# Kernel tuning notes

Hardware: AMD Instinct MI355X
Metric: run time of the kernel (lower is better)

## Reference

```python
import jax, jax.numpy as jnp
import numpy as np

EMBED = 3072
HEADS = 24
HEAD_DIM = EMBED // HEADS
FFN = 4 * EMBED
SEGS = (1024, 2048, 4096)
DILS = (1, 2, 4)
SEQ = 8192
BATCH = 1


def setup_inputs() -> dict:
    key = jax.random.key(0)
    ks = jax.random.split(key, 8)
    E, F = EMBED, FFN
    s = lambda k, shape, sc: (jax.random.normal(k, shape, jnp.float32) * sc)
    return {
        "x": s(ks[0], (BATCH, SEQ, E), 1.0),
        "expert_embed": s(ks[1], (1, 1, E), 0.02),
        "w_qkv": s(ks[2], (3 * E, E), E ** -0.5),
        "b_qkv": jnp.zeros((3 * E,), jnp.float32),
        "w_out": s(ks[3], (E, E), E ** -0.5),
        "b_out": jnp.zeros((E,), jnp.float32),
        "ln1_g": jnp.ones((E,), jnp.float32),
        "ln1_b": jnp.zeros((E,), jnp.float32),
        "w1": s(ks[4], (F, E), E ** -0.5),
        "b1": jnp.zeros((F,), jnp.float32),
        "w2": s(ks[5], (E, F), F ** -0.5),
        "b2": jnp.zeros((E,), jnp.float32),
        "ln2_g": jnp.ones((E,), jnp.float32),
        "ln2_b": jnp.zeros((E,), jnp.float32),
    }


def _layernorm(x, g, b):
    m = jnp.mean(x, axis=-1, keepdims=True)
    v = jnp.mean(jnp.square(x - m), axis=-1, keepdims=True)
    return (x - m) * jax.lax.rsqrt(v + 1e-5) * g + b


def _dilated_attn(q, k, v):
    # q,k,v: [b, n, h, d]; heads are partitioned across dilation groups
    b, n, h, d = q.shape
    G = len(SEGS)
    hg = h // G
    scale = 1.0 / np.sqrt(d)
    outs = []
    for i, (g, r) in enumerate(zip(SEGS, DILS)):
        off = i % r
        hs = slice(i * hg, (i + 1) * hg)

        def sel(t):
            # [b, n, h, d] -> [b, n//g, g//r, hg, d] (dilated segment view)
            return t.reshape(b, n // g, g, h, d)[:, :, off::r, hs, :]

        qi, ki, vi = sel(q), sel(k), sel(v)
        att = jnp.einsum("bsqhd,bskhd->bshqk", qi, ki) * scale
        att = jax.nn.softmax(att, axis=-1)
        oi = jnp.einsum("bshqk,bskhd->bsqhd", att, vi)
        # scatter dilated positions back; unselected positions stay zero
        buf = jnp.zeros((b, n // g, g, hg, d), q.dtype).at[:, :, off::r].set(oi)
        outs.append(buf.reshape(b, n, hg, d))
    return jnp.concatenate(outs, axis=2)  # head groups are contiguous slices


def reference(x, expert_embed, w_qkv, b_qkv, w_out, b_out,
              ln1_g, ln1_b, w1, b1, w2, b2, ln2_g, ln2_b):
    b, n, E = x.shape
    x = x + expert_embed
    qkv = x @ w_qkv.T + b_qkv
    q, k, v = [t.reshape(b, n, HEADS, HEAD_DIM) for t in jnp.split(qkv, 3, axis=-1)]
    a = _dilated_attn(q, k, v).reshape(b, n, E) @ w_out.T + b_out
    x = _layernorm(x + a, ln1_g, ln1_b)
    f = jax.nn.gelu(x @ w1.T + b1, approximate=False) @ w2.T + b2
    return _layernorm(x + f, ln2_g, ln2_b)
```

## Files before the change

### kernel.cpp

```cpp
#include <hip/hip_runtime.h>

typedef unsigned short u16;
typedef __bf16 bf16x8 __attribute__((ext_vector_type(8)));
typedef float f32x4 __attribute__((ext_vector_type(4)));
typedef u16 u16x4 __attribute__((ext_vector_type(4)));
typedef u16 u16x8 __attribute__((ext_vector_type(8)));

__device__ __forceinline__ u16 f2bf(float f) {
  union { float f; unsigned u; } v; v.f = f;
  return (u16)((v.u + 0x7fffu + ((v.u >> 16) & 1u)) >> 16);
}
__device__ __forceinline__ float b2f(u16 h) {
  union { unsigned u; float f; } v; v.u = ((unsigned)h) << 16; return v.f;
}

__device__ __forceinline__ void gld16(const void* g, void* l) {
  __builtin_amdgcn_global_load_lds(
      (const __attribute__((address_space(1))) unsigned int*)g,
      (__attribute__((address_space(3))) unsigned int*)l, 16, 0, 0);
}

#define BAR() asm volatile("s_barrier" ::: "memory")
#define VMC6() asm volatile("s_waitcnt vmcnt(6)" ::: "memory")
#define VMC0() asm volatile("s_waitcnt vmcnt(0)" ::: "memory")

__global__ __launch_bounds__(256) void prep_kernel(const float* __restrict__ x,
                                                   const float* __restrict__ ee,
                                                   u16* __restrict__ xb) {
  size_t i = ((size_t)blockIdx.x * 256 + threadIdx.x) * 4;
  int col = (int)(i % 3072);
  f32x4 v = *(const f32x4*)&x[i];
  f32x4 e = *(const f32x4*)&ee[col];
  v += e;
  u16x4 b = { f2bf(v[0]), f2bf(v[1]), f2bf(v[2]), f2bf(v[3]) };
  *(u16x4*)&xb[i] = b;
}

__global__ __launch_bounds__(256) void cvt_kernel(const float* __restrict__ in,
                                                  u16* __restrict__ out, size_t n) {
  size_t i = ((size_t)blockIdx.x * 256 + threadIdx.x) * 4;
  if (i >= n) return;
  f32x4 v = *(const f32x4*)&in[i];
  u16x4 b = { f2bf(v[0]), f2bf(v[1]), f2bf(v[2]), f2bf(v[3]) };
  *(u16x4*)&out[i] = b;
}

__global__ __launch_bounds__(256) void cvt_strided_kernel(const float* __restrict__ in,
                                                          u16* __restrict__ out, int k0) {
  size_t i = ((size_t)blockIdx.x * 256 + threadIdx.x) * 4;
  int n = (int)(i / 6144), k = (int)(i % 6144);
  f32x4 v = *(const f32x4*)&in[(size_t)n * 12288 + k0 + k];
  u16x4 b = { f2bf(v[0]), f2bf(v[1]), f2bf(v[2]), f2bf(v[3]) };
  *(u16x4*)&out[i] = b;
}

template<int EPI>
__global__ __launch_bounds__(512, 2) void gemm8_kernel(const u16* __restrict__ A,
                                                       const u16* __restrict__ B,
                                                       const float* __restrict__ bias,
                                                       void* __restrict__ C0,
                                                       void* __restrict__ C1,
                                                       int N, int K) {
  __shared__ __align__(16) u16 lds[65536];
  const int tid = threadIdx.x;
  const int lane = tid & 63;
  const int w = tid >> 6;
  const int lr = lane & 15, lc8 = (lane >> 4) * 8;
  const int wm128 = (w >> 2) * 128, wn64 = (w & 3) * 64;
  const int rsw = (lr & 7) << 3;

  const int ntile = N >> 8;
  int bid = blockIdx.x;
  int wg = (bid & 7) * (gridDim.x >> 3) + (bid >> 3);
  const int bm = wg / ntile, bn = wg % ntile;
  const size_t m0 = (size_t)bm << 8, n0 = (size_t)bn << 8;

  const int jsw = (tid & 7) ^ ((tid >> 3) & 7);
  const u16* gA = A + (m0 + (tid >> 3)) * (size_t)K + jsw * 8;
  const u16* gB = B + (n0 + ((tid >> 8) << 6) + ((tid >> 3) & 31)) * (size_t)K + jsw * 8;
  u16* lA = &lds[tid * 8];
  u16* lB = &lds[16384 + (((tid >> 8) << 12) | (((tid >> 3) & 31) << 6) | ((tid & 7) << 3))];

  f32x4 acc[8][4] = {};
  bf16x8 af[2][4], bfr[2][2];

  auto stageA = [&](int buf, int mh, int kk) {
    const int ro = mh * 64;
    gld16(gA + (size_t)ro * K + kk, lA + buf * 32768 + ro * 64);
    gld16(gA + (size_t)(ro + 128) * K + kk, lA + buf * 32768 + (ro + 128) * 64);
  };
  auto stageB = [&](int buf, int nh, int kk) {
    const int ro = nh * 32;
    gld16(gB + (size_t)ro * K + kk, lB + buf * 32768 + ro * 64);
    gld16(gB + (size_t)(ro + 128) * K + kk, lB + buf * 32768 + (ro + 128) * 64);
  };
  auto LA = [&](int buf, int mh) {
#pragma unroll
    for (int ks = 0; ks < 2; ++ks)
#pragma unroll
      for (int f = 0; f < 4; ++f) {
        int r = wm128 + mh * 64 + f * 16 + lr;
        af[ks][f] = *(const bf16x8*)&lds[buf * 32768 + r * 64 + ((ks * 32 + lc8) ^ rsw)];
      }
  };
  auto LB = [&](int buf, int nh) {
#pragma unroll
    for (int ks = 0; ks < 2; ++ks)
#pragma unroll
      for (int f = 0; f < 2; ++f) {
        int r = wn64 + nh * 32 + f * 16 + lr;
        bfr[ks][f] = *(const bf16x8*)&lds[buf * 32768 + 16384 + r * 64 + ((ks * 32 + lc8) ^ rsw)];
      }
  };
  auto MMA = [&](int mh, int nh) {
    __builtin_amdgcn_s_setprio(1);
#pragma unroll
    for (int ks = 0; ks < 2; ++ks)
#pragma unroll
      for (int f = 0; f < 4; ++f)
#pragma unroll
        for (int f2 = 0; f2 < 2; ++f2)
          acc[mh * 4 + f][nh * 2 + f2] = __builtin_amdgcn_mfma_f32_16x16x32_bf16(
              af[ks][f], bfr[ks][f2], acc[mh * 4 + f][nh * 2 + f2], 0, 0, 0);
    __builtin_amdgcn_s_setprio(0);
  };

  stageA(0, 0, 0); stageB(0, 1, 0); stageA(0, 1, 0); stageB(0, 0, 0);
  stageA(1, 0, 64); stageB(1, 1, 64); stageA(1, 1, 64);
  VMC6();
  BAR();

  const int NIT = K >> 7;
  for (int it = 0; it < NIT; ++it) {
    const int kk = it << 7;
    const bool pred = (it + 1 < NIT);
    LA(0, 0); LB(0, 0);
    stageB(1, 0, kk + 64);
    BAR(); MMA(0, 0); BAR();
    LB(0, 1);
    if (pred) stageA(0, 0, kk + 128);
    BAR(); MMA(0, 1); BAR();
    LA(0, 1);
    if (pred) stageB(0, 1, kk + 128);
    BAR(); MMA(1, 1); BAR();
    LB(0, 0);
    if (pred) stageA(0, 1, kk + 128);
    BAR(); MMA(1, 0);
    if (pred) { VMC6(); } else { VMC0(); }
    BAR();
    LA(1, 0); LB(1, 0);
    if (pred) stageB(0, 0, kk + 128);
    BAR(); MMA(0, 0); BAR();
    LB(1, 1);
    if (pred) stageA(1, 0, kk + 192);
    BAR(); MMA(0, 1); BAR();
    LA(1, 1);
    if (pred) stageB(1, 1, kk + 192);
    BAR(); MMA(1, 1); BAR();
    LB(1, 0);
    if (pred) stageA(1, 1, kk + 192);
    BAR(); MMA(1, 0);
    if (pred) { VMC6(); }
    BAR();
  }

#pragma unroll
  for (int ni = 0; ni < 4; ++ni) {
    const int colL = wn64 + ni * 16 + lr;
    const size_t col = n0 + colL;
    const float bv = bias[col];
    const int ci = colL >> 3;
#pragma unroll
    for (int mi = 0; mi < 8; ++mi) {
#pragma unroll
      for (int rg = 0; rg < 4; ++rg) {
        const int rowL = wm128 + mi * 16 + (lc8 >> 1) + rg;
        float v = acc[mi][ni][rg] + bv;
        if constexpr (EPI == 2)
          v = 0.5f * v * (1.0f + erff(v * 0.7071067811865476f));
        const int fz = (rowL >> 2) & 7;
        lds[rowL * 256 + (((ci ^ fz) << 3) | (colL & 7))] = f2bf(v);
      }
    }
  }
  __syncthreads();
  const int row = tid >> 1, half = tid & 1;
  const int fro = (row >> 2) & 7;
  u16* dst;
  size_t cb;
  int ldc;
  if constexpr (EPI == 7) {
    const int sec = (n0 >= 3072);
    dst = sec ? (u16*)C1 : (u16*)C0;
    cb = n0 - (sec ? 3072 : 0);
    ldc = 3072;
  } else {
    dst = (u16*)C0; cb = n0; ldc = N;
  }
  u16* gout = dst + (m0 + row) * (size_t)ldc + cb + half * 128;
#pragma unroll
  for (int i = 0; i < 16; ++i) {
    const int ci = half * 16 + i;
    *(uint4*)&gout[i * 8] = *(const uint4*)&lds[row * 256 + ((ci ^ fro) << 3)];
  }
}

template<int EPI>
__global__ __launch_bounds__(512, 2) void gemm4p_kernel(const u16* __restrict__ A,
                                                        const u16* __restrict__ B,
                                                        const float* __restrict__ bias,
                                                        const float* __restrict__ residf,
                                                        const u16* __restrict__ residb,
                                                        const float* __restrict__ ee,
                                                        void* __restrict__ C0,
                                                        int N, int K) {
  __shared__ __align__(16) u16 lds[73728];
  const int tid = threadIdx.x;
  const int lane = tid & 63;
  const int w = tid >> 6;
  const int lr = lane & 15, lc8 = (lane >> 4) * 8;
  const int wm64 = (w >> 1) * 64;
  const int wn64 = (w & 1) * 64;
  const int rsw = (lr & 7) << 3;

  const int ntile = N >> 7;
  int bid = blockIdx.x;
  int wg = (bid & 7) * (gridDim.x >> 3) + (bid >> 3);
  const int bm = wg / ntile, bn = wg % ntile;
  const size_t m0 = (size_t)bm << 8, n0 = (size_t)bn << 7;

  const int jsw = (tid & 7) ^ ((tid >> 3) & 7);
  const u16* gA = A + (m0 + (tid >> 3)) * (size_t)K + jsw * 8;
  const u16* gB = B + (n0 + (tid >> 3)) * (size_t)K + jsw * 8;
  u16* lA = &lds[tid * 8];
  u16* lB = &lds[16384 + tid * 8];

  f32x4 acc[4][4] = {};
  bf16x8 af[2][4], bfr[2][2];

  const int NT = K >> 6;

  auto stageA2 = [&](int buf, int kk) {
    gld16(gA + kk, lA + buf * 24576);
    gld16(gA + (size_t)128 * K + kk, lA + buf * 24576 + 128 * 64);
    gld16(gA + (size_t)64 * K + kk, lA + buf * 24576 + 64 * 64);
    gld16(gA + (size_t)192 * K + kk, lA + buf * 24576 + 192 * 64);
  };
  auto stageB1 = [&](int buf, int kk) {
    gld16(gB + kk, lB + buf * 24576);
    gld16(gB + (size_t)64 * K + kk, lB + buf * 24576 + 64 * 64);
  };
  auto LA = [&](int buf) {
#pragma unroll
    for (int ks = 0; ks < 2; ++ks)
#pragma unroll
      for (int f = 0; f < 4; ++f) {
        int r = wm64 + f * 16 + lr;
        af[ks][f] = *(const bf16x8*)&lds[buf * 24576 + r * 64 + ((ks * 32 + lc8) ^ rsw)];
      }
  };
  auto LB = [&](int buf, int ch) {
#pragma unroll
    for (int ks = 0; ks < 2; ++ks)
#pragma unroll
      for (int f2 = 0; f2 < 2; ++f2) {
        int r = wn64 + ch * 32 + f2 * 16 + lr;
        bfr[ks][f2] = *(const bf16x8*)&lds[buf * 24576 + 16384 + r * 64 + ((ks * 32 + lc8) ^ rsw)];
      }
  };
  auto MMA = [&](int ch) {
    __builtin_amdgcn_s_setprio(1);
#pragma unroll
    for (int ks = 0; ks < 2; ++ks)
#pragma unroll
      for (int f = 0; f < 4; ++f)
#pragma unroll
        for (int f2 = 0; f2 < 2; ++f2)
          acc[f][ch * 2 + f2] = __builtin_amdgcn_mfma_f32_16x16x32_bf16(
              af[ks][f], bfr[ks][f2], acc[f][ch * 2 + f2], 0, 0, 0);
    __builtin_amdgcn_s_setprio(0);
  };
  auto TILE = [&](int bc, int bs, int tt) {
    const int kk2 = (tt + 2) << 6;
    const bool p = (tt + 2) < NT;
    LA(bc); LB(bc, 0);
    if (p) stageA2(bs, kk2);
    BAR(); MMA(0); BAR();
    LB(bc, 1);
    if (p) stageB1(bs, kk2);
    BAR(); MMA(1);
    if (p) { VMC6(); } else { VMC0(); }
    BAR();
  };

  stageA2(0, 0); stageB1(0, 0);
  stageA2(1, 64); stageB1(1, 64);
  VMC6();
  BAR();

  for (int t = 0; t < NT; t += 3) {
    TILE(0, 2, t);
    TILE(1, 0, t + 1);
    TILE(2, 1, t + 2);
  }

#pragma unroll
  for (int nf = 0; nf < 4; ++nf) {
    const int colL = wn64 + nf * 16 + lr;
    const size_t col = n0 + colL;
    float bv = 0.f;
    if constexpr (EPI != 9) bv = bias[col];
    const int ci = colL >> 3;
#pragma unroll
    for (int f = 0; f < 4; ++f) {
#pragma unroll
      for (int rg = 0; rg < 4; ++rg) {
        const int rowL = wm64 + f * 16 + (lc8 >> 1) + rg;
        const size_t idx = (m0 + rowL) * (size_t)N + col;
        float v = acc[f][nf][rg] + bv;
        if constexpr (EPI == 3) v += residf[idx] + ee[col];
        if constexpr (EPI == 8) v += b2f(residb[idx]);
        if constexpr (EPI == 9) v += b2f(((const u16*)C0)[idx]);
        const int fz = (rowL >> 2) & 7;
        lds[rowL * 128 + (((ci ^ fz) << 3) | (colL & 7))] = f2bf(v);
      }
    }
  }
  __syncthreads();
  const int row = tid >> 1, half = tid & 1;
  const int fro = (row >> 2) & 7;
  u16* gout = (u16*)C0 + (m0 + row) * (size_t)N + n0 + half * 64;
#pragma unroll
  for (int i = 0; i < 8; ++i) {
    const int ci = half * 8 + i;
    *(uint4*)&gout[i * 8] = *(const uint4*)&lds[row * 128 + ((ci ^ fro) << 3)];
  }
}

__device__ __forceinline__ void decode_blk(int bid, int& grp, int& g, int& r, int& off,
                                           int& q16, int& hl, int& s) {
  if (bid < 1024)      { grp = 0; g = 1024; r = 1; off = 0; }
  else if (bid < 1536) { grp = 1; g = 2048; r = 2; off = 1; bid -= 1024; }
  else                 { grp = 2; g = 4096; r = 4; off = 2; bid -= 1536; }
  q16 = bid & 15; hl = (bid >> 4) & 7; s = bid >> 7;
}

__global__ __launch_bounds__(256) void vtrans_kernel(const u16* __restrict__ Vb,
                                                     u16* __restrict__ vtd) {
  int grp, g, r, off, jb, hl, s;
  decode_blk(blockIdx.x, grp, g, r, off, jb, hl, s);
  const int h = grp * 8 + hl;
  const size_t vbase = (size_t)((grp == 0) ? 0u : (grp == 1) ? 8388608u : 12582912u)
                       + (size_t)(s * 8 + hl) * 131072;
  __shared__ u16 t[64 * 128];
  const int tid = threadIdx.x;
#pragma unroll
  for (int i = 0; i < 4; ++i) {
    int c = tid + i * 256;
    int jj = c >> 4, c16 = c & 15;
    size_t pos = (size_t)s * g + off + (size_t)(jb * 64 + jj) * r;
    uint4 d = *(const uint4*)&Vb[pos * 3072 + h * 128 + c16 * 8];
    *(uint4*)((char*)t + jj * 256 + ((c16 * 16) ^ ((jj >> 3) << 4))) = d;
  }
  __syncthreads();
#pragma unroll
  for (int i = 0; i < 4; ++i) {
    int c = tid + i * 256;
    int dd = c >> 3, jc = c & 7;
    u16x8 vals;
#pragma unroll
    for (int q = 0; q < 8; ++q) {
      int row = jc * 8 + q;
      vals[q] = *(const u16*)((const char*)t + row * 256 + ((dd * 2) ^ (jc << 4)));
    }
    *(u16x8*)&vtd[vbase + (size_t)dd * 1024 + jb * 64 + jc * 8] = vals;
  }
}

__global__ __launch_bounds__(256) void attn_kernel(const u16* __restrict__ Qb,
                                                   const u16* __restrict__ Kb,
                                                   const u16* __restrict__ vtd,
                                                   u16* __restrict__ abuf) {
  int grp, g, r, off, qt, hl, s;
  decode_blk(blockIdx.x, grp, g, r, off, qt, hl, s);
  const int h = grp * 8 + hl;
  const size_t vbase = (size_t)((grp == 0) ? 0u : (grp == 1) ? 8388608u : 12582912u)
                       + (size_t)(s * 8 + hl) * 131072;
  const size_t segoff = (size_t)s * g + off;

  const int tid = threadIdx.x;
  const int lane = tid & 63, w = tid >> 6;
  const int lr = lane & 15, lc = lane >> 4;

  __shared__ u16 Kl[64 * 128];
  __shared__ u16 Vl[128 * 64];
  __shared__ u16 Pl[4][1024];

  const size_t qpos = segoff + (size_t)(qt * 64 + w * 16 + lr) * r;
  const u16* qrow = &Qb[qpos * 3072 + h * 128];
  bf16x8 qf[4];
#pragma unroll
  for (int kc = 0; kc < 4; ++kc) qf[kc] = *(const bf16x8*)&qrow[kc * 32 + lc * 8];

  float m_run[4], l_run[4];
  f32x4 ao[8] = {};
#pragma unroll
  for (int i = 0; i < 4; ++i) { m_run[i] = -1e30f; l_run[i] = 0.f; }

  const float scale = 0.08838834764831845f;

  for (int kt = 0; kt < 16; ++kt) {
    __syncthreads();
#pragma unroll
    for (int i = 0; i < 4; ++i) {
      int c = tid + i * 256;
      int jj = c >> 4, c16 = c & 15;
      size_t kpos = segoff + (size_t)(kt * 64 + jj) * r;
      uint4 kd = *(const uint4*)&Kb[kpos * 3072 + h * 128 + c16 * 8];
      *(uint4*)((char*)Kl + jj * 256 + ((c16 * 16) ^ ((jj & 7) << 4))) = kd;
      int dd = c >> 3, jc = c & 7;
      uint4 vd = *(const uint4*)&vtd[vbase + (size_t)dd * 1024 + kt * 64 + jc * 8];
      *(uint4*)((char*)Vl + dd * 128 + ((jc * 16) ^ ((dd & 7) << 4))) = vd;
    }
    __syncthreads();

    f32x4 sc4[4] = {};
#pragma unroll
    for (int kb = 0; kb < 4; ++kb) {
      const int key = kb * 16 + lr;
      const int swz = (key & 7) << 4;
#pragma unroll
      for (int kc = 0; kc < 4; ++kc) {
        bf16x8 kf = *(const bf16x8*)((const char*)Kl + key * 256 + ((kc * 64 + lc * 16) ^ swz));
        sc4[kb] = __builtin_amdgcn_mfma_f32_16x16x32_bf16(qf[kc], kf, sc4[kb], 0, 0, 0);
      }
    }

    float pv[4][4];
#pragma unroll
    for (int rg = 0; rg < 4; ++rg) {
      float t = fmaxf(fmaxf(sc4[0][rg], sc4[1][rg]), fmaxf(sc4[2][rg], sc4[3][rg]));
#pragma unroll
      for (int sh = 1; sh < 16; sh <<= 1) t = fmaxf(t, __shfl_xor(t, sh, 64));
      t *= scale;
      const float mn = fmaxf(m_run[rg], t);
      const float corr = __expf(m_run[rg] - mn);
      m_run[rg] = mn;
      float sum = 0.f;
#pragma unroll
      for (int kb = 0; kb < 4; ++kb) {
        float p = __expf(sc4[kb][rg] * scale - mn);
        pv[kb][rg] = p; sum += p;
      }
#pragma unroll
      for (int sh = 1; sh < 16; sh <<= 1) sum += __shfl_xor(sum, sh, 64);
      l_run[rg] = l_run[rg] * corr + sum;
#pragma unroll
      for (int nb = 0; nb < 8; ++nb) ao[nb][rg] *= corr;
    }

#pragma unroll
    for (int rg = 0; rg < 4; ++rg) {
      const int q = lc * 4 + rg;
      const int swq = (q & 7) << 4;
#pragma unroll
      for (int kb = 0; kb < 4; ++kb) {
        const int key = kb * 16 + lr;
        *(u16*)((char*)&Pl[w][0] + q * 128 + ((key * 2) ^ swq)) = f2bf(pv[kb][rg]);
      }
    }
    __syncthreads();

#pragma unroll
    for (int kc2 = 0; kc2 < 2; ++kc2) {
      bf16x8 pf = *(const bf16x8*)((const char*)&Pl[w][0] + lr * 128 + ((kc2 * 64 + lc * 16) ^ ((lr & 7) << 4)));
#pragma unroll
      for (int nb = 0; nb < 8; ++nb) {
        const int dd = nb * 16 + lr;
        bf16x8 vf = *(const bf16x8*)((const char*)Vl + dd * 128 + ((kc2 * 64 + lc * 16) ^ ((dd & 7) << 4)));
        ao[nb] = __builtin_amdgcn_mfma_f32_16x16x32_bf16(pf, vf, ao[nb], 0, 0, 0);
      }
    }
  }

#pragma unroll
  for (int rg = 0; rg < 4; ++rg) {
    const float inv = 1.f / l_run[rg];
    const size_t opos = segoff + (size_t)(qt * 64 + w * 16 + lc * 4 + rg) * r;
    u16* orow = &abuf[opos * 3072 + h * 128];
#pragma unroll
    for (int nb = 0; nb < 8; ++nb) orow[nb * 16 + lr] = f2bf(ao[nb][rg] * inv);
  }
}

template<int IN_BF, int OUT_BF>
__global__ __launch_bounds__(256) void ln_kernel(const void* __restrict__ yv,
                                                 const float* __restrict__ gm,
                                                 const float* __restrict__ bt,
                                                 void* __restrict__ outv) {
  const size_t row = blockIdx.x;
  const int tid = threadIdx.x;
  float v[12];
  float s = 0.f, ss = 0.f;
#pragma unroll
  for (int i = 0; i < 3; ++i) {
    if constexpr (IN_BF) {
      u16x4 raw = *(const u16x4*)((const u16*)yv + row * 3072 + tid * 4 + i * 1024);
#pragma unroll
      for (int j = 0; j < 4; ++j) { float f = b2f(raw[j]); v[i * 4 + j] = f; s += f; ss += f * f; }
    } else {
      f32x4 raw = *(const f32x4*)((const float*)yv + row * 3072 + tid * 4 + i * 1024);
#pragma unroll
      for (int j = 0; j < 4; ++j) { float f = raw[j]; v[i * 4 + j] = f; s += f; ss += f * f; }
    }
  }
#pragma unroll
  for (int sh = 1; sh < 64; sh <<= 1) { s += __shfl_xor(s, sh, 64); ss += __shfl_xor(ss, sh, 64); }
  __shared__ float red[8];
  if ((tid & 63) == 0) { red[tid >> 6] = s; red[4 + (tid >> 6)] = ss; }
  __syncthreads();
  s = red[0] + red[1] + red[2] + red[3];
  ss = red[4] + red[5] + red[6] + red[7];
  const float mean = s * (1.f / 3072.f);
  const float var = ss * (1.f / 3072.f) - mean * mean;
  const float rs = rsqrtf(var + 1e-5f);
#pragma unroll
  for (int i = 0; i < 3; ++i) {
    int c = tid * 4 + i * 1024;
    f32x4 g4 = *(const f32x4*)&gm[c];
    f32x4 b4 = *(const f32x4*)&bt[c];
    if constexpr (OUT_BF) {
      u16x4 ob;
#pragma unroll
      for (int j = 0; j < 4; ++j) ob[j] = f2bf((v[i * 4 + j] - mean) * rs * g4[j] + b4[j]);
      *(u16x4*)((u16*)outv + row * 3072 + c) = ob;
    } else {
      f32x4 o;
#pragma unroll
      for (int j = 0; j < 4; ++j) o[j] = (v[i * 4 + j] - mean) * rs * g4[j] + b4[j];
      *(f32x4*)((float*)outv + row * 3072 + c) = o;
    }
  }
}

extern "C" void kernel_launch(void* const* d_in, const int* in_sizes, int n_in,
                              void* d_out, int out_size, void* d_ws, size_t ws_size,
                              hipStream_t stream) {
  (void)in_sizes; (void)n_in; (void)out_size;
  const float* x    = (const float*)d_in[0];
  const float* ee   = (const float*)d_in[1];
  const float* wqkv = (const float*)d_in[2];
  const float* bqkv = (const float*)d_in[3];
  const float* wout = (const float*)d_in[4];
  const float* bout = (const float*)d_in[5];
  const float* ln1g = (const float*)d_in[6];
  const float* ln1b = (const float*)d_in[7];
  const float* w1   = (const float*)d_in[8];
  const float* b1   = (const float*)d_in[9];
  const float* w2   = (const float*)d_in[10];
  const float* b2   = (const float*)d_in[11];
  const float* ln2g = (const float*)d_in[12];
  const float* ln2b = (const float*)d_in[13];
  float* out = (float*)d_out;

  static const size_t OFF_B1  = 50331648;
  static const size_t OFF_B2  = 100663296;
  static const size_t WS_NEED = 150994944;
  if (ws_size < WS_NEED) return;

  char* ws = (char*)d_ws;
  u16*   xb    = (u16*)(ws);
  u16*   vtd   = (u16*)(ws);
  u16*   wbo   = (u16*)(ws);
  u16*   x1b   = (u16*)(ws);
  u16*   Qb    = (u16*)(ws + OFF_B1);
  u16*   y1b   = (u16*)(ws + OFF_B1);
  u16*   y2b   = (u16*)(ws + OFF_B1);
  u16*   wslot = (u16*)(ws + OFF_B2);
  u16*   abuf  = (u16*)(ws + OFF_B2);
  u16*   Kb    = (u16*)d_out;
  u16*   Vb    = (u16*)((char*)d_out + 50331648);
  u16*   hcd   = (u16*)d_out;

  prep_kernel<<<24576, 256, 0, stream>>>(x, ee, xb);

  cvt_kernel<<<18432, 256, 0, stream>>>(wqkv, wslot, 18874368);
  gemm8_kernel<7><<<768, 512, 0, stream>>>(xb, wslot, bqkv, Qb, Kb, 6144, 3072);
  cvt_kernel<<<9216, 256, 0, stream>>>(wqkv + 18874368, wslot, 9437184);
  gemm4p_kernel<0><<<768, 512, 0, stream>>>(xb, wslot, bqkv + 6144, nullptr, nullptr, nullptr,
                                            Vb, 3072, 3072);

  vtrans_kernel<<<1792, 256, 0, stream>>>(Vb, vtd);
  hipMemsetAsync(abuf, 0, 50331648, stream);
  attn_kernel<<<1792, 256, 0, stream>>>(Qb, Kb, vtd, abuf);

  cvt_kernel<<<9216, 256, 0, stream>>>(wout, wbo, 9437184);
  gemm4p_kernel<3><<<768, 512, 0, stream>>>(abuf, wbo, bout, x, nullptr, ee,
                                            y1b, 3072, 3072);
  ln_kernel<1, 1><<<8192, 256, 0, stream>>>(y1b, ln1g, ln1b, x1b);

  for (int c = 0; c < 2; ++c) {
    cvt_kernel<<<18432, 256, 0, stream>>>(w1 + (size_t)c * 18874368, wslot, 18874368);
    gemm8_kernel<2><<<768, 512, 0, stream>>>(x1b, wslot, b1 + c * 6144, hcd, nullptr, 6144, 3072);
    cvt_strided_kernel<<<18432, 256, 0, stream>>>(w2, wslot, c * 6144);
    if (c == 0)
      gemm4p_kernel<8><<<768, 512, 0, stream>>>(hcd, wslot, b2, nullptr, x1b, nullptr,
                                                y2b, 3072, 6144);
    else
      gemm4p_kernel<9><<<768, 512, 0, stream>>>(hcd, wslot, b2, nullptr, nullptr, nullptr,
                                                y2b, 3072, 6144);
  }

  ln_kernel<1, 0><<<8192, 256, 0, stream>>>(y2b, ln2g, ln2b, out);
}
```

Before: 2.253 ms.

## Restructure GEMM pipelines to load full B fragment and halve barrier phases

Both GEMM kernels now load the whole per-wave B fragment at once and issue larger MFMA blocks per phase. This halves the number of barrier-separated sub-steps per K-tile, and the staging order and vmcnt waits are reorganised to match. In the 256x256 kernel the LDS layout moves to separate A and B regions. The goal is to cut barrier and LDS-read scheduling overhead, at the cost of more live fragment registers and a changed pipeline depth that could expose memory latency or create races.

```diff
diff --git a/kernel.cpp b/kernel.cpp
--- a/kernel.cpp
+++ b/kernel.cpp
@@ -21,7 +21,9 @@
 }
 
 #define BAR() asm volatile("s_barrier" ::: "memory")
+#define VMC8() asm volatile("s_waitcnt vmcnt(8)" ::: "memory")
 #define VMC6() asm volatile("s_waitcnt vmcnt(6)" ::: "memory")
+#define VMC2() asm volatile("s_waitcnt vmcnt(2)" ::: "memory")
 #define VMC0() asm volatile("s_waitcnt vmcnt(0)" ::: "memory")
 
 __global__ __launch_bounds__(256) void prep_kernel(const float* __restrict__ x,
@@ -79,20 +81,20 @@
   const u16* gA = A + (m0 + (tid >> 3)) * (size_t)K + jsw * 8;
   const u16* gB = B + (n0 + ((tid >> 8) << 6) + ((tid >> 3) & 31)) * (size_t)K + jsw * 8;
   u16* lA = &lds[tid * 8];
-  u16* lB = &lds[16384 + (((tid >> 8) << 12) | (((tid >> 3) & 31) << 6) | ((tid & 7) << 3))];
+  u16* lB = &lds[32768 + (((tid >> 8) << 12) | (((tid >> 3) & 31) << 6) | ((tid & 7) << 3))];
 
   f32x4 acc[8][4] = {};
-  bf16x8 af[2][4], bfr[2][2];
+  bf16x8 af[2][4], bfr[2][4];
 
   auto stageA = [&](int buf, int mh, int kk) {
     const int ro = mh * 64;
-    gld16(gA + (size_t)ro * K + kk, lA + buf * 32768 + ro * 64);
-    gld16(gA + (size_t)(ro + 128) * K + kk, lA + buf * 32768 + (ro + 128) * 64);
+    gld16(gA + (size_t)ro * K + kk, lA + buf * 16384 + ro * 64);
+    gld16(gA + (size_t)(ro + 128) * K + kk, lA + buf * 16384 + (ro + 128) * 64);
   };
   auto stageB = [&](int buf, int nh, int kk) {
     const int ro = nh * 32;
-    gld16(gB + (size_t)ro * K + kk, lB + buf * 32768 + ro * 64);
-    gld16(gB + (size_t)(ro + 128) * K + kk, lB + buf * 32768 + (ro + 128) * 64);
+    gld16(gB + (size_t)ro * K + kk, lB + buf * 16384 + ro * 64);
+    gld16(gB + (size_t)(ro + 128) * K + kk, lB + buf * 16384 + (ro + 128) * 64);
   };
   auto LA = [&](int buf, int mh) {
 #pragma unroll
@@ -100,67 +102,58 @@
 #pragma unroll
       for (int f = 0; f < 4; ++f) {
         int r = wm128 + mh * 64 + f * 16 + lr;
-        af[ks][f] = *(const bf16x8*)&lds[buf * 32768 + r * 64 + ((ks * 32 + lc8) ^ rsw)];
-      }
-  };
-  auto LB = [&](int buf, int nh) {
+        af[ks][f] = *(const bf16x8*)&lds[buf * 16384 + r * 64 + ((ks * 32 + lc8) ^ rsw)];
+      }
+  };
+  auto LBall = [&](int buf) {
 #pragma unroll
     for (int ks = 0; ks < 2; ++ks)
 #pragma unroll
-      for (int f = 0; f < 2; ++f) {
-        int r = wn64 + nh * 32 + f * 16 + lr;
-        bfr[ks][f] = *(const bf16x8*)&lds[buf * 32768 + 16384 + r * 64 + ((ks * 32 + lc8) ^ rsw)];
-      }
-  };
-  auto MMA = [&](int mh, int nh) {
+      for (int f = 0; f < 4; ++f) {
+        int r = wn64 + f * 16 + lr;
+        bfr[ks][f] = *(const bf16x8*)&lds[32768 + buf * 16384 + r * 64 + ((ks * 32 + lc8) ^ rsw)];
+      }
+  };
+  auto MMA = [&](int mh) {
     __builtin_amdgcn_s_setprio(1);
 #pragma unroll
     for (int ks = 0; ks < 2; ++ks)
 #pragma unroll
       for (int f = 0; f < 4; ++f)
 #pragma unroll
-        for (int f2 = 0; f2 < 2; ++f2)
-          acc[mh * 4 + f][nh * 2 + f2] = __builtin_amdgcn_mfma_f32_16x16x32_bf16(
-              af[ks][f], bfr[ks][f2], acc[mh * 4 + f][nh * 2 + f2], 0, 0, 0);
+        for (int f2 = 0; f2 < 4; ++f2)
+          acc[mh * 4 + f][f2] = __builtin_amdgcn_mfma_f32_16x16x32_bf16(
+              af[ks][f], bfr[ks][f2], acc[mh * 4 + f][f2], 0, 0, 0);
     __builtin_amdgcn_s_setprio(0);
   };
 
-  stageA(0, 0, 0); stageB(0, 1, 0); stageA(0, 1, 0); stageB(0, 0, 0);
-  stageA(1, 0, 64); stageB(1, 1, 64); stageA(1, 1, 64);
-  VMC6();
+  stageB(0, 0, 0); stageB(0, 1, 0); stageA(0, 0, 0);
+  stageA(0, 1, 0);
+  stageB(1, 0, 64); stageB(1, 1, 64); stageA(1, 0, 64);
+  VMC8();
   BAR();
 
   const int NIT = K >> 7;
   for (int it = 0; it < NIT; ++it) {
     const int kk = it << 7;
     const bool pred = (it + 1 < NIT);
-    LA(0, 0); LB(0, 0);
-    stageB(1, 0, kk + 64);
-    BAR(); MMA(0, 0); BAR();
-    LB(0, 1);
-    if (pred) stageA(0, 0, kk + 128);
-    BAR(); MMA(0, 1); BAR();
+    LBall(0); LA(0, 0);
+    stageA(1, 1, kk + 64);
+    BAR(); MMA(0); VMC8(); BAR();
     LA(0, 1);
-    if (pred) stageB(0, 1, kk + 128);
-    BAR(); MMA(1, 1); BAR();
-    LB(0, 0);
+    if (pred) { stageB(0, 0, kk + 128); stageB(0, 1, kk + 128); stageA(0, 0, kk + 128); }
+    BAR(); MMA(1);
+    if (pred) { VMC8(); } else { VMC2(); }
+    BAR();
+    LBall(1); LA(1, 0);
     if (pred) stageA(0, 1, kk + 128);
-    BAR(); MMA(1, 0);
-    if (pred) { VMC6(); } else { VMC0(); }
+    BAR(); MMA(0);
+    if (pred) { VMC8(); } else { VMC0(); }
     BAR();
-    LA(1, 0); LB(1, 0);
-    if (pred) stageB(0, 0, kk + 128);
-    BAR(); MMA(0, 0); BAR();
-    LB(1, 1);
-    if (pred) stageA(1, 0, kk + 192);
-    BAR(); MMA(0, 1); BAR();
     LA(1, 1);
-    if (pred) stageB(1, 1, kk + 192);
-    BAR(); MMA(1, 1); BAR();
-    LB(1, 0);
-    if (pred) stageA(1, 1, kk + 192);
-    BAR(); MMA(1, 0);
-    if (pred) { VMC6(); }
+    if (pred) { stageB(1, 0, kk + 192); stageB(1, 1, kk + 192); stageA(1, 0, kk + 192); }
+    BAR(); MMA(1);
+    if (pred) { VMC8(); }
     BAR();
   }
 
@@ -206,7 +199,7 @@
 }
 
 template<int EPI>
-__global__ __launch_bounds__(512, 2) void gemm4p_kernel(const u16* __restrict__ A,
+__global__ __launch_bounds__(512, 2) void gemm1p_kernel(const u16* __restrict__ A,
                                                         const u16* __restrict__ B,
                                                         const float* __restrict__ bias,
                                                         const float* __restrict__ residf,
@@ -236,17 +229,17 @@
   u16* lB = &lds[16384 + tid * 8];
 
   f32x4 acc[4][4] = {};
-  bf16x8 af[2][4], bfr[2][2];
+  bf16x8 af[2][4], bfr[2][4];
 
   const int NT = K >> 6;
 
   auto stageA2 = [&](int buf, int kk) {
     gld16(gA + kk, lA + buf * 24576);
+    gld16(gA + (size_t)64 * K + kk, lA + buf * 24576 + 64 * 64);
     gld16(gA + (size_t)128 * K + kk, lA + buf * 24576 + 128 * 64);
-    gld16(gA + (size_t)64 * K + kk, lA + buf * 24576 + 64 * 64);
     gld16(gA + (size_t)192 * K + kk, lA + buf * 24576 + 192 * 64);
   };
-  auto stageB1 = [&](int buf, int kk) {
+  auto stageB2 = [&](int buf, int kk) {
     gld16(gB + kk, lB + buf * 24576);
     gld16(gB + (size_t)64 * K + kk, lB + buf * 24576 + 64 * 64);
   };
@@ -259,42 +252,39 @@
         af[ks][f] = *(const bf16x8*)&lds[buf * 24576 + r * 64 + ((ks * 32 + lc8) ^ rsw)];
       }
   };
-  auto LB = [&](int buf, int ch) {
+  auto LBall = [&](int buf) {
 #pragma unroll
     for (int ks = 0; ks < 2; ++ks)
 #pragma unroll
-      for (int f2 = 0; f2 < 2; ++f2) {
-        int r = wn64 + ch * 32 + f2 * 16 + lr;
-        bfr[ks][f2] = *(const bf16x8*)&lds[buf * 24576 + 16384 + r * 64 + ((ks * 32 + lc8) ^ rsw)];
-      }
-  };
-  auto MMA = [&](int ch) {
+      for (int f = 0; f < 4; ++f) {
+        int r = wn64 + f * 16 + lr;
+        bfr[ks][f] = *(const bf16x8*)&lds[buf * 24576 + 16384 + r * 64 + ((ks * 32 + lc8) ^ rsw)];
+      }
+  };
+  auto MMA = [&]() {
     __builtin_amdgcn_s_setprio(1);
 #pragma unroll
     for (int ks = 0; ks < 2; ++ks)
 #pragma unroll
       for (int f = 0; f < 4; ++f)
 #pragma unroll
-        for (int f2 = 0; f2 < 2; ++f2)
-          acc[f][ch * 2 + f2] = __builtin_amdgcn_mfma_f32_16x16x32_bf16(
-              af[ks][f], bfr[ks][f2], acc[f][ch * 2 + f2], 0, 0, 0);
+        for (int f2 = 0; f2 < 4; ++f2)
+          acc[f][f2] = __builtin_amdgcn_mfma_f32_16x16x32_bf16(
+              af[ks][f], bfr[ks][f2], acc[f][f2], 0, 0, 0);
     __builtin_amdgcn_s_setprio(0);
   };
   auto TILE = [&](int bc, int bs, int tt) {
     const int kk2 = (tt + 2) << 6;
     const bool p = (tt + 2) < NT;
-    LA(bc); LB(bc, 0);
-    if (p) stageA2(bs, kk2);
-    BAR(); MMA(0); BAR();
-    LB(bc, 1);
-    if (p) stageB1(bs, kk2);
-    BAR(); MMA(1);
+    LA(bc); LBall(bc);
+    if (p) { stageA2(bs, kk2); stageB2(bs, kk2); }
+    BAR(); MMA();
     if (p) { VMC6(); } else { VMC0(); }
     BAR();
   };
 
-  stageA2(0, 0); stageB1(0, 0);
-  stageA2(1, 64); stageB1(1, 64);
+  stageA2(0, 0); stageB2(0, 0);
+  stageA2(1, 64); stageB2(1, 64);
   VMC6();
   BAR();
 
@@ -587,7 +577,7 @@
   cvt_kernel<<<18432, 256, 0, stream>>>(wqkv, wslot, 18874368);
   gemm8_kernel<7><<<768, 512, 0, stream>>>(xb, wslot, bqkv, Qb, Kb, 6144, 3072);
   cvt_kernel<<<9216, 256, 0, stream>>>(wqkv + 18874368, wslot, 9437184);
-  gemm4p_kernel<0><<<768, 512, 0, stream>>>(xb, wslot, bqkv + 6144, nullptr, nullptr, nullptr,
+  gemm1p_kernel<0><<<768, 512, 0, stream>>>(xb, wslot, bqkv + 6144, nullptr, nullptr, nullptr,
                                             Vb, 3072, 3072);
 
   vtrans_kernel<<<1792, 256, 0, stream>>>(Vb, vtd);
@@ -595,7 +585,7 @@
   attn_kernel<<<1792, 256, 0, stream>>>(Qb, Kb, vtd, abuf);
 
   cvt_kernel<<<9216, 256, 0, stream>>>(wout, wbo, 9437184);
-  gemm4p_kernel<3><<<768, 512, 0, stream>>>(abuf, wbo, bout, x, nullptr, ee,
+  gemm1p_kernel<3><<<768, 512, 0, stream>>>(abuf, wbo, bout, x, nullptr, ee,
                                             y1b, 3072, 3072);
   ln_kernel<1, 1><<<8192, 256, 0, stream>>>(y1b, ln1g, ln1b, x1b);
 
@@ -604,10 +594,10 @@
     gemm8_kernel<2><<<768, 512, 0, stream>>>(x1b, wslot, b1 + c * 6144, hcd, nullptr, 6144, 3072);
     cvt_strided_kernel<<<18432, 256, 0, stream>>>(w2, wslot, c * 6144);
     if (c == 0)
-      gemm4p_kernel<8><<<768, 512, 0, stream>>>(hcd, wslot, b2, nullptr, x1b, nullptr,
+      gemm1p_kernel<8><<<768, 512, 0, stream>>>(hcd, wslot, b2, nullptr, x1b, nullptr,
                                                 y2b, 3072, 6144);
     else
-      gemm4p_kernel<9><<<768, 512, 0, stream>>>(hcd, wslot, b2, nullptr, nullptr, nullptr,
+      gemm1p_kernel<9><<<768, 512, 0, stream>>>(hcd, wslot, b2, nullptr, nullptr, nullptr,
                                                 y2b, 3072, 6144);
   }
 
```

New measurement: 2.318 ms. 2.9% more time.

## Merge split MMA phases in 4-phase GEMM and reorder gemm8 prefetch schedule

Applied to the files above, without the earlier changes.

The 256x128 GEMM now loads all B fragments per k-tile and issues a single MMA block with one barrier per tile instead of two half-tile phases separated by barriers. The 8-wave GEMM reorders which A/B stages are prefetched in each phase and tightens the vmcnt wait from 6 to 4 outstanding loads. The aim is to cut barrier stalls and better align global loads with their consumers. Costs are higher register pressure from the larger B fragment array and less interleaving of LDS reads with MFMA work.

```diff
diff --git a/kernel.cpp b/kernel.cpp
--- a/kernel.cpp
+++ b/kernel.cpp
@@ -21,6 +21,7 @@
 }
 
 #define BAR() asm volatile("s_barrier" ::: "memory")
+#define VMC4() asm volatile("s_waitcnt vmcnt(4)" ::: "memory")
 #define VMC6() asm volatile("s_waitcnt vmcnt(6)" ::: "memory")
 #define VMC0() asm volatile("s_waitcnt vmcnt(0)" ::: "memory")
 
@@ -126,8 +127,8 @@
   };
 
   stageA(0, 0, 0); stageB(0, 1, 0); stageA(0, 1, 0); stageB(0, 0, 0);
-  stageA(1, 0, 64); stageB(1, 1, 64); stageA(1, 1, 64);
-  VMC6();
+  stageA(1, 0, 64); stageB(1, 1, 64);
+  VMC4();
   BAR();
 
   const int NIT = K >> 7;
@@ -135,32 +136,32 @@
     const int kk = it << 7;
     const bool pred = (it + 1 < NIT);
     LA(0, 0); LB(0, 0);
-    stageB(1, 0, kk + 64);
+    stageA(1, 1, kk + 64);
     BAR(); MMA(0, 0); BAR();
     LB(0, 1);
-    if (pred) stageA(0, 0, kk + 128);
+    stageB(1, 0, kk + 64);
     BAR(); MMA(0, 1); BAR();
     LA(0, 1);
-    if (pred) stageB(0, 1, kk + 128);
+    if (pred) stageA(0, 0, kk + 128);
     BAR(); MMA(1, 1); BAR();
     LB(0, 0);
-    if (pred) stageA(0, 1, kk + 128);
+    if (pred) stageB(0, 1, kk + 128);
     BAR(); MMA(1, 0);
-    if (pred) { VMC6(); } else { VMC0(); }
+    if (pred) { VMC4(); } else { VMC0(); }
     BAR();
     LA(1, 0); LB(1, 0);
-    if (pred) stageB(0, 0, kk + 128);
+    if (pred) stageA(0, 1, kk + 128);
     BAR(); MMA(0, 0); BAR();
     LB(1, 1);
-    if (pred) stageA(1, 0, kk + 192);
+    if (pred) stageB(0, 0, kk + 128);
     BAR(); MMA(0, 1); BAR();
     LA(1, 1);
-    if (pred) stageB(1, 1, kk + 192);
+    if (pred) stageA(1, 0, kk + 192);
     BAR(); MMA(1, 1); BAR();
     LB(1, 0);
-    if (pred) stageA(1, 1, kk + 192);
+    if (pred) stageB(1, 1, kk + 192);
     BAR(); MMA(1, 0);
-    if (pred) { VMC6(); }
+    if (pred) { VMC4(); }
     BAR();
   }
 
@@ -206,14 +207,14 @@
 }
 
 template<int EPI>
-__global__ __launch_bounds__(512, 2) void gemm4p_kernel(const u16* __restrict__ A,
-                                                        const u16* __restrict__ B,
-                                                        const float* __restrict__ bias,
-                                                        const float* __restrict__ residf,
-                                                        const u16* __restrict__ residb,
-                                                        const float* __restrict__ ee,
-                                                        void* __restrict__ C0,
-                                                        int N, int K) {
+__global__ __launch_bounds__(512, 2) void gemmu_kernel(const u16* __restrict__ A,
+                                                       const u16* __restrict__ B,
+                                                       const float* __restrict__ bias,
+                                                       const float* __restrict__ residf,
+                                                       const u16* __restrict__ residb,
+                                                       const float* __restrict__ ee,
+                                                       void* __restrict__ C0,
+                                                       int N, int K) {
   __shared__ __align__(16) u16 lds[73728];
   const int tid = threadIdx.x;
   const int lane = tid & 63;
@@ -236,17 +237,17 @@
   u16* lB = &lds[16384 + tid * 8];
 
   f32x4 acc[4][4] = {};
-  bf16x8 af[2][4], bfr[2][2];
+  bf16x8 af[2][4], bfr[2][4];
 
   const int NT = K >> 6;
 
   auto stageA2 = [&](int buf, int kk) {
     gld16(gA + kk, lA + buf * 24576);
+    gld16(gA + (size_t)64 * K + kk, lA + buf * 24576 + 64 * 64);
     gld16(gA + (size_t)128 * K + kk, lA + buf * 24576 + 128 * 64);
-    gld16(gA + (size_t)64 * K + kk, lA + buf * 24576 + 64 * 64);
     gld16(gA + (size_t)192 * K + kk, lA + buf * 24576 + 192 * 64);
   };
-  auto stageB1 = [&](int buf, int kk) {
+  auto stageB2 = [&](int buf, int kk) {
     gld16(gB + kk, lB + buf * 24576);
     gld16(gB + (size_t)64 * K + kk, lB + buf * 24576 + 64 * 64);
   };
@@ -259,42 +260,39 @@
         af[ks][f] = *(const bf16x8*)&lds[buf * 24576 + r * 64 + ((ks * 32 + lc8) ^ rsw)];
       }
   };
-  auto LB = [&](int buf, int ch) {
+  auto LBall = [&](int buf) {
 #pragma unroll
     for (int ks = 0; ks < 2; ++ks)
 #pragma unroll
-      for (int f2 = 0; f2 < 2; ++f2) {
-        int r = wn64 + ch * 32 + f2 * 16 + lr;
-        bfr[ks][f2] = *(const bf16x8*)&lds[buf * 24576 + 16384 + r * 64 + ((ks * 32 + lc8) ^ rsw)];
-      }
-  };
-  auto MMA = [&](int ch) {
+      for (int f = 0; f < 4; ++f) {
+        int r = wn64 + f * 16 + lr;
+        bfr[ks][f] = *(const bf16x8*)&lds[buf * 24576 + 16384 + r * 64 + ((ks * 32 + lc8) ^ rsw)];
+      }
+  };
+  auto MMA = [&]() {
     __builtin_amdgcn_s_setprio(1);
 #pragma unroll
     for (int ks = 0; ks < 2; ++ks)
 #pragma unroll
       for (int f = 0; f < 4; ++f)
 #pragma unroll
-        for (int f2 = 0; f2 < 2; ++f2)
-          acc[f][ch * 2 + f2] = __builtin_amdgcn_mfma_f32_16x16x32_bf16(
-              af[ks][f], bfr[ks][f2], acc[f][ch * 2 + f2], 0, 0, 0);
+        for (int f2 = 0; f2 < 4; ++f2)
+          acc[f][f2] = __builtin_amdgcn_mfma_f32_16x16x32_bf16(
+              af[ks][f], bfr[ks][f2], acc[f][f2], 0, 0, 0);
     __builtin_amdgcn_s_setprio(0);
   };
   auto TILE = [&](int bc, int bs, int tt) {
     const int kk2 = (tt + 2) << 6;
     const bool p = (tt + 2) < NT;
-    LA(bc); LB(bc, 0);
-    if (p) stageA2(bs, kk2);
-    BAR(); MMA(0); BAR();
-    LB(bc, 1);
-    if (p) stageB1(bs, kk2);
-    BAR(); MMA(1);
+    LA(bc); LBall(bc);
+    if (p) { stageA2(bs, kk2); stageB2(bs, kk2); }
+    MMA();
     if (p) { VMC6(); } else { VMC0(); }
     BAR();
   };
 
-  stageA2(0, 0); stageB1(0, 0);
-  stageA2(1, 64); stageB1(1, 64);
+  stageA2(0, 0); stageB2(0, 0);
+  stageA2(1, 64); stageB2(1, 64);
   VMC6();
   BAR();
 
@@ -587,16 +585,16 @@
   cvt_kernel<<<18432, 256, 0, stream>>>(wqkv, wslot, 18874368);
   gemm8_kernel<7><<<768, 512, 0, stream>>>(xb, wslot, bqkv, Qb, Kb, 6144, 3072);
   cvt_kernel<<<9216, 256, 0, stream>>>(wqkv + 18874368, wslot, 9437184);
-  gemm4p_kernel<0><<<768, 512, 0, stream>>>(xb, wslot, bqkv + 6144, nullptr, nullptr, nullptr,
-                                            Vb, 3072, 3072);
+  gemmu_kernel<0><<<768, 512, 0, stream>>>(xb, wslot, bqkv + 6144, nullptr, nullptr, nullptr,
+                                           Vb, 3072, 3072);
 
   vtrans_kernel<<<1792, 256, 0, stream>>>(Vb, vtd);
   hipMemsetAsync(abuf, 0, 50331648, stream);
   attn_kernel<<<1792, 256, 0, stream>>>(Qb, Kb, vtd, abuf);
 
   cvt_kernel<<<9216, 256, 0, stream>>>(wout, wbo, 9437184);
-  gemm4p_kernel<3><<<768, 512, 0, stream>>>(abuf, wbo, bout, x, nullptr, ee,
-                                            y1b, 3072, 3072);
+  gemmu_kernel<3><<<768, 512, 0, stream>>>(abuf, wbo, bout, x, nullptr, ee,
+                                           y1b, 3072, 3072);
   ln_kernel<1, 1><<<8192, 256, 0, stream>>>(y1b, ln1g, ln1b, x1b);
 
   for (int c = 0; c < 2; ++c) {
@@ -604,11 +602,11 @@
     gemm8_kernel<2><<<768, 512, 0, stream>>>(x1b, wslot, b1 + c * 6144, hcd, nullptr, 6144, 3072);
     cvt_strided_kernel<<<18432, 256, 0, stream>>>(w2, wslot, c * 6144);
     if (c == 0)
-      gemm4p_kernel<8><<<768, 512, 0, stream>>>(hcd, wslot, b2, nullptr, x1b, nullptr,
-                                                y2b, 3072, 6144);
+      gemmu_kernel<8><<<768, 512, 0, stream>>>(hcd, wslot, b2, nullptr, x1b, nullptr,
+                                               y2b, 3072, 6144);
     else
-      gemm4p_kernel<9><<<768, 512, 0, stream>>>(hcd, wslot, b2, nullptr, nullptr, nullptr,
-                                                y2b, 3072, 6144);
+      gemmu_kernel<9><<<768, 512, 0, stream>>>(hcd, wslot, b2, nullptr, nullptr, nullptr,
+                                               y2b, 3072, 6144);
   }
 
   ln_kernel<1, 0><<<8192, 256, 0, stream>>>(y2b, ln2g, ln2b, out);
```

Result: no change. 2.238 ms (-0.7%).
